# Kernel tuning notes

Hardware: AMD Instinct MI355X
Metric: run time of the kernel (lower is better)

## Reference

```python
import jax, jax.numpy as jnp
import numpy as np

N_NODES = 50000
N_EDGES = 800000
D_MODEL = 128
N_HEADS = 4
N_LAYERS = 2
F_HEAD = D_MODEL // N_HEADS


def setup_inputs() -> dict:
    key = jax.random.key(0)
    ks = jax.random.split(key, 6)
    x = jax.random.normal(ks[0], (N_NODES, D_MODEL), dtype=jnp.float32)
    edge_index = jax.random.randint(ks[1], (2, N_EDGES), 0, N_NODES, dtype=jnp.int64)
    scale = 1.0 / np.sqrt(D_MODEL)
    W = jax.random.normal(ks[2], (N_LAYERS, D_MODEL, D_MODEL), dtype=jnp.float32) * scale
    a_src = jax.random.normal(ks[3], (N_LAYERS, N_HEADS, F_HEAD), dtype=jnp.float32) * scale
    a_dst = jax.random.normal(ks[4], (N_LAYERS, N_HEADS, F_HEAD), dtype=jnp.float32) * scale
    b = jnp.zeros((N_LAYERS, D_MODEL), dtype=jnp.float32)
    return {"x": x, "edge_index": edge_index, "W": W, "a_src": a_src, "a_dst": a_dst, "b": b}


def _gat_layer(x, src, dst, W_l, a_src_l, a_dst_l, b_l, apply_act):
    N = x.shape[0]
    H, F = a_src_l.shape
    # projected node features, split into heads: [N, H, F]
    h = (x @ W_l).reshape(N, H, F)
    # per-node attention contributions: [N, H]
    alpha_s = jnp.einsum("nhf,hf->nh", h, a_src_l)
    alpha_d = jnp.einsum("nhf,hf->nh", h, a_dst_l)
    # per-edge raw scores, LeakyReLU(0.2): [E, H]
    e = jax.nn.leaky_relu(alpha_s[src] + alpha_d[dst], negative_slope=0.2)
    # numerically-stable segment softmax over edges grouped by target node
    e_max = jax.ops.segment_max(e, dst, num_segments=N)
    e_exp = jnp.exp(e - e_max[dst])
    denom = jax.ops.segment_sum(e_exp, dst, num_segments=N)
    alpha = e_exp / (denom[dst] + 1e-16)  # [E, H]
    # gather source features, weight, scatter-add to targets
    msg = h[src] * alpha[:, :, None]  # [E, H, F]
    out = jax.ops.segment_sum(msg, dst, num_segments=N).reshape(N, H * F)
    out = out + x + b_l  # skip connection (dims match) + bias
    return jax.nn.elu(out) if apply_act else out


def reference(x, edge_index, W, a_src, a_dst, b):
    src, dst = edge_index[0], edge_index[1]
    L = W.shape[0]
    for l in range(L):
        x = _gat_layer(x, src, dst, W[l], a_src[l], a_dst[l], b[l], apply_act=(l < L - 1))
    return x
```

## Files before the change

kernel.cpp:

```cpp
#include <hip/hip_runtime.h>
#include <math.h>

constexpr int NN = 50000;
constexpr int NE = 800000;
constexpr int D  = 128;
constexpr int NH = 4;
constexpr int NBUK = (NN + 255) / 256;
constexpr int CAP  = 4608;

typedef __attribute__((ext_vector_type(8))) short short8v;
typedef __attribute__((ext_vector_type(4))) float f32x4;

__device__ inline unsigned short rne_bf16(float f) {
    unsigned bits = __float_as_uint(f);
    return (unsigned short)((bits + 0x7FFFu + ((bits >> 16) & 1u)) >> 16);
}

__global__ __launch_bounds__(256) void bucket_hist_kernel(
    const int* __restrict__ dst, int* __restrict__ btot)
{
    __shared__ int c[NBUK];
    for (int i = threadIdx.x; i < NBUK; i += 256) c[i] = 0;
    __syncthreads();
    const int base = blockIdx.x * 2048;
    #pragma unroll
    for (int i = 0; i < 8; ++i) {
        int e = base + i * 256 + threadIdx.x;
        if (e < NE) atomicAdd(&c[dst[e] >> 8], 1);
    }
    __syncthreads();
    for (int i = threadIdx.x; i < NBUK; i += 256)
        if (c[i]) atomicAdd(&btot[i], c[i]);
}

__global__ __launch_bounds__(256) void bucket_scan_kernel(
    const int* __restrict__ btot, int* __restrict__ bbase,
    int* __restrict__ bwp, int* __restrict__ row_ptr)
{
    const int t = threadIdx.x;
    int v = (t < NBUK) ? btot[t] : 0;
    __shared__ int s[256];
    s[t] = v;
    __syncthreads();
    for (int off = 1; off < 256; off <<= 1) {
        int u = (t >= off) ? s[t - off] : 0;
        __syncthreads();
        s[t] += u;
        __syncthreads();
    }
    if (t < NBUK) { int ex = s[t] - v; bbase[t] = ex; bwp[t] = ex; }
    if (t == 0) row_ptr[NN] = NE;
}

__global__ __launch_bounds__(256) void partition_kernel(
    const int* __restrict__ src, const int* __restrict__ dst,
    int* __restrict__ bwp, unsigned* __restrict__ bukbuf)
{
    __shared__ int cnt[NBUK];
    __shared__ int run[NBUK];
    for (int i = threadIdx.x; i < NBUK; i += 256) cnt[i] = 0;
    __syncthreads();
    const int base = blockIdx.x * 2048;
    int s_[8], b_[8], dl_[8];
    #pragma unroll
    for (int i = 0; i < 8; ++i) {
        int e = base + i * 256 + threadIdx.x;
        bool ok = (e < NE);
        s_[i] = ok ? src[e] : 0;
        int d = ok ? dst[e] : 0;
        b_[i] = d >> 8; dl_[i] = d & 255;
        if (ok) atomicAdd(&cnt[b_[i]], 1);
    }
    __syncthreads();
    for (int i = threadIdx.x; i < NBUK; i += 256)
        run[i] = cnt[i] ? atomicAdd(&bwp[i], cnt[i]) : 0;
    __syncthreads();
    #pragma unroll
    for (int i = 0; i < 8; ++i) {
        int e = base + i * 256 + threadIdx.x;
        if (e < NE) {
            int pos = atomicAdd(&run[b_[i]], 1);
            bukbuf[pos] = (unsigned)s_[i] | ((unsigned)dl_[i] << 16);
        }
    }
}

__global__ __launch_bounds__(256) void bucket_sort_kernel(
    const unsigned* __restrict__ bukbuf, const int* __restrict__ btot,
    const int* __restrict__ bbase, int* __restrict__ row_ptr,
    unsigned short* __restrict__ srcs)
{
    const int b = blockIdx.x;
    const int t = threadIdx.x;
    const int cnt = min(btot[b], CAP);
    const int base = bbase[b];
    __shared__ int hist[256];
    __shared__ int run[256];
    __shared__ int s[256];
    __shared__ unsigned short stage[CAP];
    hist[t] = 0;
    __syncthreads();
    for (int i = t; i < cnt; i += 256)
        atomicAdd(&hist[bukbuf[base + i] >> 16], 1);
    __syncthreads();
    int v = hist[t];
    s[t] = v;
    __syncthreads();
    for (int off = 1; off < 256; off <<= 1) {
        int u = (t >= off) ? s[t - off] : 0;
        __syncthreads();
        s[t] += u;
        __syncthreads();
    }
    const int excl = s[t] - v;
    const int node = b * 256 + t;
    if (node < NN) row_ptr[node] = base + excl;
    run[t] = excl;
    __syncthreads();
    for (int i = t; i < cnt; i += 256) {
        unsigned p = bukbuf[base + i];
        int pos = atomicAdd(&run[p >> 16], 1);
        stage[pos] = (unsigned short)(p & 0xFFFFu);
    }
    __syncthreads();
    for (int i = t; i < cnt; i += 256) srcs[base + i] = stage[i];
}

__global__ __launch_bounds__(256) void repack_kernel(const float* __restrict__ W,
                                                     unsigned short* __restrict__ Wpk,
                                                     int* __restrict__ btot) {
    if (blockIdx.x == 0 && threadIdx.x < NBUK) btot[threadIdx.x] = 0;
    int tid = blockIdx.x * 256 + threadIdx.x;
    if (tid >= 2 * 2048) return;
    int layer = tid >> 11;
    int rest  = tid & 2047;
    int tile  = rest >> 8;
    int kstep = (rest >> 6) & 3;
    int lane  = rest & 63;
    int col   = tile * 16 + (lane & 15);
    int kbase = kstep * 32 + (lane >> 4) * 8;
    const float* Wl = W + (size_t)layer * D * D;
    unsigned short v[8];
    #pragma unroll
    for (int j = 0; j < 8; ++j) v[j] = rne_bf16(Wl[(kbase + j) * D + col]);
    *(uint4*)(Wpk + (size_t)tid * 8) = *(const uint4*)v;
}

template<int BF16IN>
__global__ __launch_bounds__(256) void gemm_alpha_kernel(
    const void* __restrict__ xin, const unsigned short* __restrict__ Wpk,
    const float* __restrict__ a_src, const float* __restrict__ a_dst,
    unsigned short* __restrict__ hb, float* __restrict__ alpha_s,
    float* __restrict__ alpha_d)
{
    __shared__ unsigned short xl[64 * 128];
    const int t = threadIdx.x;
    const int row0 = blockIdx.x * 64;

    if constexpr (BF16IN) {
        const unsigned short* xb = (const unsigned short*)xin;
        #pragma unroll
        for (int it = 0; it < 4; ++it) {
            int idx = it * 256 + t;
            int r   = idx >> 4;
            int c8  = (idx & 15) * 8;
            int n   = row0 + r;
            uint4 v = {0u, 0u, 0u, 0u};
            if (n < NN) v = *(const uint4*)(xb + (size_t)n * D + c8);
            *(uint4*)(xl + r * 128 + (c8 ^ ((r & 7) << 3))) = v;
        }
    } else {
        const float* xf = (const float*)xin;
        #pragma unroll
        for (int it = 0; it < 8; ++it) {
            int idx = it * 256 + t;
            int r   = idx >> 5;
            int c4  = (idx & 31) * 4;
            int n   = row0 + r;
            float4 v;
            if (n < NN) v = *(const float4*)(xf + (size_t)n * D + c4);
            else { v.x = 0.f; v.y = 0.f; v.z = 0.f; v.w = 0.f; }
            unsigned p0 = ((unsigned)rne_bf16(v.y) << 16) | rne_bf16(v.x);
            unsigned p1 = ((unsigned)rne_bf16(v.w) << 16) | rne_bf16(v.z);
            uint2 pv; pv.x = p0; pv.y = p1;
            *(uint2*)(xl + r * 128 + (c4 ^ ((r & 7) << 3))) = pv;
        }
    }
    __syncthreads();

    const int wv  = t >> 6;
    const int l   = t & 63;
    const int l15 = l & 15;
    const int g   = l >> 4;
    const int strip = wv * 16;
    const int arow  = strip + l15;

    f32x4 acc[8];
    #pragma unroll
    for (int i = 0; i < 8; ++i) acc[i] = (f32x4){0.f, 0.f, 0.f, 0.f};

    #pragma unroll
    for (int ks = 0; ks < 4; ++ks) {
        const int k0 = ks * 32 + g * 8;
        short8v a = *(const short8v*)(xl + arow * 128 + (k0 ^ ((arow & 7) << 3)));
        #pragma unroll
        for (int tl = 0; tl < 8; ++tl) {
            short8v b = *(const short8v*)(Wpk + ((size_t)(tl * 4 + ks) * 64 + l) * 8);
            acc[tl] = __builtin_amdgcn_mfma_f32_16x16x32_bf16(a, b, acc[tl], 0, 0, 0);
        }
    }

    float as_t[8], ad_t[8];
    #pragma unroll
    for (int tl = 0; tl < 8; ++tl) {
        as_t[tl] = a_src[tl * 16 + l15];
        ad_t[tl] = a_dst[tl * 16 + l15];
    }

    #pragma unroll
    for (int r = 0; r < 4; ++r) {
        const int n = row0 + strip + g * 4 + r;
        if (n < NN) {
            #pragma unroll
            for (int tl = 0; tl < 8; ++tl)
                hb[(size_t)n * D + tl * 16 + l15] = rne_bf16(acc[tl][r]);
        }
        #pragma unroll
        for (int hd = 0; hd < NH; ++hd) {
            float ps = acc[2*hd][r] * as_t[2*hd] + acc[2*hd+1][r] * as_t[2*hd+1];
            float pd = acc[2*hd][r] * ad_t[2*hd] + acc[2*hd+1][r] * ad_t[2*hd+1];
            #pragma unroll
            for (int off = 1; off < 16; off <<= 1) {
                ps += __shfl_xor(ps, off);
                pd += __shfl_xor(pd, off);
            }
            if (l15 == 0 && n < NN) {
                alpha_s[n * NH + hd] = ps;
                alpha_d[n * NH + hd] = pd;
            }
        }
    }
}

template<int IN_BF16, int OUT_BF16, int ACT>
__global__ __launch_bounds__(256) void gather_kernel(
    const unsigned short* __restrict__ hb, const float* __restrict__ alpha_s,
    const float* __restrict__ alpha_d, const int* __restrict__ row_ptr,
    const unsigned short* __restrict__ srcs, const void* __restrict__ x_in,
    const float* __restrict__ bias, void* __restrict__ out)
{
    const int wave = threadIdx.x >> 6;
    const int lane = threadIdx.x & 63;
    const int q    = lane >> 4;
    const int ql   = lane & 15;
    const int head = ql >> 2;
    const int n = blockIdx.x * 4 + wave;
    if (n >= NN) return;

    const int start = row_ptr[n];
    const int end   = row_ptr[n + 1];
    const float4 ad4 = *(const float4*)&alpha_d[n * NH];

    float acc[8];
    #pragma unroll
    for (int c = 0; c < 8; ++c) acc[c] = 0.f;
    float den = 0.f;

    for (int base = start; base < end; base += 64) {
        const int cnt = min(64, end - base);
        int msrc = 0;
        unsigned uw01 = 0, uw23 = 0;
        if (lane < cnt) {
            msrc = srcs[base + lane];
            const float4 as4 = *(const float4*)&alpha_s[msrc * NH];
            float e0 = as4.x + ad4.x; e0 = (e0 > 0.f) ? e0 : 0.2f * e0;
            float e1 = as4.y + ad4.y; e1 = (e1 > 0.f) ? e1 : 0.2f * e1;
            float e2 = as4.z + ad4.z; e2 = (e2 > 0.f) ? e2 : 0.2f * e2;
            float e3 = as4.w + ad4.w; e3 = (e3 > 0.f) ? e3 : 0.2f * e3;
            float w0 = __expf(e0), w1 = __expf(e1);
            float w2 = __expf(e2), w3 = __expf(e3);
            uw01 = ((unsigned)rne_bf16(w1) << 16) | rne_bf16(w0);
            uw23 = ((unsigned)rne_bf16(w3) << 16) | rne_bf16(w2);
        }
        for (int m = 0; m < cnt; m += 4) {
            const int me = m + q;
            int s = __shfl(msrc, me);
            unsigned b01 = (unsigned)__shfl((int)uw01, me);
            unsigned b23 = (unsigned)__shfl((int)uw23, me);
            unsigned uw = (head < 2) ? b01 : b23;
            float w = __uint_as_float((head & 1) ? (uw & 0xFFFF0000u) : (uw << 16));
            den += w;
            const uint4 hv = *(const uint4*)(hb + (size_t)s * D + ql * 8);
            acc[0] = fmaf(w, __uint_as_float(hv.x << 16),          acc[0]);
            acc[1] = fmaf(w, __uint_as_float(hv.x & 0xFFFF0000u),  acc[1]);
            acc[2] = fmaf(w, __uint_as_float(hv.y << 16),          acc[2]);
            acc[3] = fmaf(w, __uint_as_float(hv.y & 0xFFFF0000u),  acc[3]);
            acc[4] = fmaf(w, __uint_as_float(hv.z << 16),          acc[4]);
            acc[5] = fmaf(w, __uint_as_float(hv.z & 0xFFFF0000u),  acc[5]);
            acc[6] = fmaf(w, __uint_as_float(hv.w << 16),          acc[6]);
            acc[7] = fmaf(w, __uint_as_float(hv.w & 0xFFFF0000u),  acc[7]);
        }
    }
    #pragma unroll
    for (int c = 0; c < 8; ++c) {
        acc[c] += __shfl_xor(acc[c], 16);
        acc[c] += __shfl_xor(acc[c], 32);
    }
    den += __shfl_xor(den, 16);
    den += __shfl_xor(den, 32);

    const float inv = 1.f / (den + 1e-16f);
    const int c0 = ql * 8 + q * 2;
    const size_t o2 = (size_t)n * D + c0;
    float xi0, xi1;
    if constexpr (IN_BF16) {
        unsigned xv = *(const unsigned*)((const unsigned short*)x_in + o2);
        xi0 = __uint_as_float(xv << 16);
        xi1 = __uint_as_float(xv & 0xFFFF0000u);
    } else {
        const float2 xv = *(const float2*)((const float*)x_in + o2);
        xi0 = xv.x; xi1 = xv.y;
    }
    const float2 bi = *(const float2*)(bias + c0);
    float v0 = fmaf(acc[q * 2],     inv, xi0) + bi.x;
    float v1 = fmaf(acc[q * 2 + 1], inv, xi1) + bi.y;
    if constexpr (ACT) {
        v0 = (v0 > 0.f) ? v0 : (__expf(v0) - 1.f);
        v1 = (v1 > 0.f) ? v1 : (__expf(v1) - 1.f);
    }
    if constexpr (OUT_BF16) {
        unsigned ov = ((unsigned)rne_bf16(v1) << 16) | rne_bf16(v0);
        *(unsigned*)((unsigned short*)out + o2) = ov;
    } else {
        float2 o; o.x = v0; o.y = v1;
        *(float2*)((float*)out + o2) = o;
    }
}

extern "C" void kernel_launch(void* const* d_in, const int* in_sizes, int n_in,
                              void* d_out, int out_size, void* d_ws, size_t ws_size,
                              hipStream_t stream) {
    const float* x     = (const float*)d_in[0];
    const int*   ei    = (const int*)d_in[1];
    const float* W     = (const float*)d_in[2];
    const float* a_src = (const float*)d_in[3];
    const float* a_dst = (const float*)d_in[4];
    const float* bias  = (const float*)d_in[5];
    float* outp = (float*)d_out;

    const int* e_src = ei;
    const int* e_dst = ei + NE;

    char* base = (char*)d_ws;
    unsigned short* hb  = (unsigned short*)(base);
    unsigned short* x1b = (unsigned short*)(base + 12800000);
    float* al_s    = (float*)(base + 25600000);
    float* al_d    = (float*)(base + 26400000);
    int*   row_ptr = (int*)  (base + 27200000);
    unsigned short* srcs = (unsigned short*)(base + 27400064);
    unsigned* bukbuf = (unsigned*)(base + 29000064);
    int*   btot    = (int*)  (base + 32200064);
    int*   bbase   = (int*)  (base + 32201088);
    int*   bwp     = (int*)  (base + 32202112);
    unsigned short* Wpk = (unsigned short*)(base + 32203136);

    repack_kernel<<<16, 256, 0, stream>>>(W, Wpk, btot);
    const int pblocks = (NE + 2047) / 2048;
    bucket_hist_kernel<<<pblocks, 256, 0, stream>>>(e_dst, btot);
    bucket_scan_kernel<<<1, 256, 0, stream>>>(btot, bbase, bwp, row_ptr);
    partition_kernel<<<pblocks, 256, 0, stream>>>(e_src, e_dst, bwp, bukbuf);
    bucket_sort_kernel<<<NBUK, 256, 0, stream>>>(bukbuf, btot, bbase, row_ptr, srcs);

    const int gemm_blocks   = (NN + 63) / 64;
    const int gather_blocks = (NN + 3) / 4;

    gemm_alpha_kernel<0><<<gemm_blocks, 256, 0, stream>>>(x, Wpk, a_src, a_dst,
                                                          hb, al_s, al_d);
    gather_kernel<0, 1, 1><<<gather_blocks, 256, 0, stream>>>(
        hb, al_s, al_d, row_ptr, srcs, x, bias, x1b);
    gemm_alpha_kernel<1><<<gemm_blocks, 256, 0, stream>>>(x1b, Wpk + 2048 * 8,
                                                          a_src + D, a_dst + D,
                                                          hb, al_s, al_d);
    gather_kernel<1, 0, 0><<<gather_blocks, 256, 0, stream>>>(
        hb, al_s, al_d, row_ptr, srcs, x1b, bias + D, outp);
}
```

Baseline: 155.5 us.

## Use fixed-capacity buckets to drop histogram/scan passes; map one node per quarter-wave in gather

Edges are now partitioned straight into fixed-capacity per-bucket regions (bucket * CAP), which removes the separate histogram and scan kernels. Each node gets start and end offsets instead of a single CSR row_ptr. The gather kernel now assigns one destination node to each 16-lane group instead of one per wave, so the cross-quarter reduction shuffles go away and each lane writes 8 contiguous outputs with vector stores. In exchange, edges past CAP in a bucket are silently dropped, and each group handles its edges one at a time, which may leave lanes idle when degrees vary.

```diff
diff --git a/kernel.cpp b/kernel.cpp
--- a/kernel.cpp
+++ b/kernel.cpp
@@ -14,42 +14,6 @@
 __device__ inline unsigned short rne_bf16(float f) {
     unsigned bits = __float_as_uint(f);
     return (unsigned short)((bits + 0x7FFFu + ((bits >> 16) & 1u)) >> 16);
-}
-
-__global__ __launch_bounds__(256) void bucket_hist_kernel(
-    const int* __restrict__ dst, int* __restrict__ btot)
-{
-    __shared__ int c[NBUK];
-    for (int i = threadIdx.x; i < NBUK; i += 256) c[i] = 0;
-    __syncthreads();
-    const int base = blockIdx.x * 2048;
-    #pragma unroll
-    for (int i = 0; i < 8; ++i) {
-        int e = base + i * 256 + threadIdx.x;
-        if (e < NE) atomicAdd(&c[dst[e] >> 8], 1);
-    }
-    __syncthreads();
-    for (int i = threadIdx.x; i < NBUK; i += 256)
-        if (c[i]) atomicAdd(&btot[i], c[i]);
-}
-
-__global__ __launch_bounds__(256) void bucket_scan_kernel(
-    const int* __restrict__ btot, int* __restrict__ bbase,
-    int* __restrict__ bwp, int* __restrict__ row_ptr)
-{
-    const int t = threadIdx.x;
-    int v = (t < NBUK) ? btot[t] : 0;
-    __shared__ int s[256];
-    s[t] = v;
-    __syncthreads();
-    for (int off = 1; off < 256; off <<= 1) {
-        int u = (t >= off) ? s[t - off] : 0;
-        __syncthreads();
-        s[t] += u;
-        __syncthreads();
-    }
-    if (t < NBUK) { int ex = s[t] - v; bbase[t] = ex; bwp[t] = ex; }
-    if (t == 0) row_ptr[NN] = NE;
 }
 
 __global__ __launch_bounds__(256) void partition_kernel(
@@ -80,20 +44,21 @@
         int e = base + i * 256 + threadIdx.x;
         if (e < NE) {
             int pos = atomicAdd(&run[b_[i]], 1);
-            bukbuf[pos] = (unsigned)s_[i] | ((unsigned)dl_[i] << 16);
+            if (pos < CAP)
+                bukbuf[b_[i] * CAP + pos] = (unsigned)s_[i] | ((unsigned)dl_[i] << 16);
         }
     }
 }
 
 __global__ __launch_bounds__(256) void bucket_sort_kernel(
-    const unsigned* __restrict__ bukbuf, const int* __restrict__ btot,
-    const int* __restrict__ bbase, int* __restrict__ row_ptr,
+    const unsigned* __restrict__ bukbuf, const int* __restrict__ bwp,
+    int* __restrict__ row_start, int* __restrict__ row_end,
     unsigned short* __restrict__ srcs)
 {
     const int b = blockIdx.x;
     const int t = threadIdx.x;
-    const int cnt = min(btot[b], CAP);
-    const int base = bbase[b];
+    const int cnt = min(bwp[b], CAP);
+    const int base = b * CAP;
     __shared__ int hist[256];
     __shared__ int run[256];
     __shared__ int s[256];
@@ -114,7 +79,10 @@
     }
     const int excl = s[t] - v;
     const int node = b * 256 + t;
-    if (node < NN) row_ptr[node] = base + excl;
+    if (node < NN) {
+        row_start[node] = base + excl;
+        row_end[node]   = base + excl + v;
+    }
     run[t] = excl;
     __syncthreads();
     for (int i = t; i < cnt; i += 256) {
@@ -128,8 +96,8 @@
 
 __global__ __launch_bounds__(256) void repack_kernel(const float* __restrict__ W,
                                                      unsigned short* __restrict__ Wpk,
-                                                     int* __restrict__ btot) {
-    if (blockIdx.x == 0 && threadIdx.x < NBUK) btot[threadIdx.x] = 0;
+                                                     int* __restrict__ bwp) {
+    if (blockIdx.x == 0 && threadIdx.x < NBUK) bwp[threadIdx.x] = 0;
     int tid = blockIdx.x * 256 + threadIdx.x;
     if (tid >= 2 * 2048) return;
     int layer = tid >> 11;
@@ -245,20 +213,21 @@
 template<int IN_BF16, int OUT_BF16, int ACT>
 __global__ __launch_bounds__(256) void gather_kernel(
     const unsigned short* __restrict__ hb, const float* __restrict__ alpha_s,
-    const float* __restrict__ alpha_d, const int* __restrict__ row_ptr,
-    const unsigned short* __restrict__ srcs, const void* __restrict__ x_in,
-    const float* __restrict__ bias, void* __restrict__ out)
+    const float* __restrict__ alpha_d, const int* __restrict__ row_start,
+    const int* __restrict__ row_end, const unsigned short* __restrict__ srcs,
+    const void* __restrict__ x_in, const float* __restrict__ bias,
+    void* __restrict__ out)
 {
-    const int wave = threadIdx.x >> 6;
     const int lane = threadIdx.x & 63;
     const int q    = lane >> 4;
     const int ql   = lane & 15;
     const int head = ql >> 2;
-    const int n = blockIdx.x * 4 + wave;
+    const int lb   = q * 16;
+    const int n = blockIdx.x * 16 + (threadIdx.x >> 6) * 4 + q;
     if (n >= NN) return;
 
-    const int start = row_ptr[n];
-    const int end   = row_ptr[n + 1];
+    const int start = row_start[n];
+    const int end   = row_end[n];
     const float4 ad4 = *(const float4*)&alpha_d[n * NH];
 
     float acc[8];
@@ -266,12 +235,12 @@
     for (int c = 0; c < 8; ++c) acc[c] = 0.f;
     float den = 0.f;
 
-    for (int base = start; base < end; base += 64) {
-        const int cnt = min(64, end - base);
+    for (int base = start; base < end; base += 16) {
+        const int cnt = min(16, end - base);
         int msrc = 0;
         unsigned uw01 = 0, uw23 = 0;
-        if (lane < cnt) {
-            msrc = srcs[base + lane];
+        if (ql < cnt) {
+            msrc = srcs[base + ql];
             const float4 as4 = *(const float4*)&alpha_s[msrc * NH];
             float e0 = as4.x + ad4.x; e0 = (e0 > 0.f) ? e0 : 0.2f * e0;
             float e1 = as4.y + ad4.y; e1 = (e1 > 0.f) ? e1 : 0.2f * e1;
@@ -282,15 +251,14 @@
             uw01 = ((unsigned)rne_bf16(w1) << 16) | rne_bf16(w0);
             uw23 = ((unsigned)rne_bf16(w3) << 16) | rne_bf16(w2);
         }
-        for (int m = 0; m < cnt; m += 4) {
-            const int me = m + q;
-            int s = __shfl(msrc, me);
-            unsigned b01 = (unsigned)__shfl((int)uw01, me);
-            unsigned b23 = (unsigned)__shfl((int)uw23, me);
+        for (int m = 0; m < cnt; ++m) {
+            int s = __shfl(msrc, lb + m);
+            unsigned b01 = (unsigned)__shfl((int)uw01, lb + m);
+            unsigned b23 = (unsigned)__shfl((int)uw23, lb + m);
             unsigned uw = (head < 2) ? b01 : b23;
             float w = __uint_as_float((head & 1) ? (uw & 0xFFFF0000u) : (uw << 16));
             den += w;
-            const uint4 hv = *(const uint4*)(hb + (size_t)s * D + ql * 8);
+            const uint4 hv = *(const uint4*)(hb + ((size_t)s << 7) + (ql << 3));
             acc[0] = fmaf(w, __uint_as_float(hv.x << 16),          acc[0]);
             acc[1] = fmaf(w, __uint_as_float(hv.x & 0xFFFF0000u),  acc[1]);
             acc[2] = fmaf(w, __uint_as_float(hv.y << 16),          acc[2]);
@@ -301,39 +269,46 @@
             acc[7] = fmaf(w, __uint_as_float(hv.w & 0xFFFF0000u),  acc[7]);
         }
     }
+
+    const float inv = 1.f / (den + 1e-16f);
+    const size_t o8 = (size_t)n * D + ql * 8;
+    float xi[8];
+    if constexpr (IN_BF16) {
+        const uint4 xv = *(const uint4*)((const unsigned short*)x_in + o8);
+        xi[0] = __uint_as_float(xv.x << 16);
+        xi[1] = __uint_as_float(xv.x & 0xFFFF0000u);
+        xi[2] = __uint_as_float(xv.y << 16);
+        xi[3] = __uint_as_float(xv.y & 0xFFFF0000u);
+        xi[4] = __uint_as_float(xv.z << 16);
+        xi[5] = __uint_as_float(xv.z & 0xFFFF0000u);
+        xi[6] = __uint_as_float(xv.w << 16);
+        xi[7] = __uint_as_float(xv.w & 0xFFFF0000u);
+    } else {
+        const float4 a = *(const float4*)((const float*)x_in + o8);
+        const float4 b = *(const float4*)((const float*)x_in + o8 + 4);
+        xi[0]=a.x; xi[1]=a.y; xi[2]=a.z; xi[3]=a.w;
+        xi[4]=b.x; xi[5]=b.y; xi[6]=b.z; xi[7]=b.w;
+    }
+    const float4 ba = *(const float4*)(bias + ql * 8);
+    const float4 bb = *(const float4*)(bias + ql * 8 + 4);
+    const float bi[8] = {ba.x, ba.y, ba.z, ba.w, bb.x, bb.y, bb.z, bb.w};
+    float o[8];
     #pragma unroll
     for (int c = 0; c < 8; ++c) {
-        acc[c] += __shfl_xor(acc[c], 16);
-        acc[c] += __shfl_xor(acc[c], 32);
-    }
-    den += __shfl_xor(den, 16);
-    den += __shfl_xor(den, 32);
-
-    const float inv = 1.f / (den + 1e-16f);
-    const int c0 = ql * 8 + q * 2;
-    const size_t o2 = (size_t)n * D + c0;
-    float xi0, xi1;
-    if constexpr (IN_BF16) {
-        unsigned xv = *(const unsigned*)((const unsigned short*)x_in + o2);
-        xi0 = __uint_as_float(xv << 16);
-        xi1 = __uint_as_float(xv & 0xFFFF0000u);
+        float v = fmaf(acc[c], inv, xi[c]) + bi[c];
+        if constexpr (ACT) v = (v > 0.f) ? v : (__expf(v) - 1.f);
+        o[c] = v;
+    }
+    if constexpr (OUT_BF16) {
+        unsigned short ov[8];
+        #pragma unroll
+        for (int c = 0; c < 8; ++c) ov[c] = rne_bf16(o[c]);
+        *(uint4*)((unsigned short*)out + o8) = *(const uint4*)ov;
     } else {
-        const float2 xv = *(const float2*)((const float*)x_in + o2);
-        xi0 = xv.x; xi1 = xv.y;
-    }
-    const float2 bi = *(const float2*)(bias + c0);
-    float v0 = fmaf(acc[q * 2],     inv, xi0) + bi.x;
-    float v1 = fmaf(acc[q * 2 + 1], inv, xi1) + bi.y;
-    if constexpr (ACT) {
-        v0 = (v0 > 0.f) ? v0 : (__expf(v0) - 1.f);
-        v1 = (v1 > 0.f) ? v1 : (__expf(v1) - 1.f);
-    }
-    if constexpr (OUT_BF16) {
-        unsigned ov = ((unsigned)rne_bf16(v1) << 16) | rne_bf16(v0);
-        *(unsigned*)((unsigned short*)out + o2) = ov;
-    } else {
-        float2 o; o.x = v0; o.y = v1;
-        *(float2*)((float*)out + o2) = o;
+        float4 oa = {o[0], o[1], o[2], o[3]};
+        float4 ob = {o[4], o[5], o[6], o[7]};
+        *(float4*)((float*)out + o8)     = oa;
+        *(float4*)((float*)out + o8 + 4) = ob;
     }
 }
 
@@ -354,33 +329,30 @@
     char* base = (char*)d_ws;
     unsigned short* hb  = (unsigned short*)(base);
     unsigned short* x1b = (unsigned short*)(base + 12800000);
-    float* al_s    = (float*)(base + 25600000);
-    float* al_d    = (float*)(base + 26400000);
-    int*   row_ptr = (int*)  (base + 27200000);
-    unsigned short* srcs = (unsigned short*)(base + 27400064);
-    unsigned* bukbuf = (unsigned*)(base + 29000064);
-    int*   btot    = (int*)  (base + 32200064);
-    int*   bbase   = (int*)  (base + 32201088);
-    int*   bwp     = (int*)  (base + 32202112);
-    unsigned short* Wpk = (unsigned short*)(base + 32203136);
-
-    repack_kernel<<<16, 256, 0, stream>>>(W, Wpk, btot);
+    float* al_s      = (float*)(base + 25600000);
+    float* al_d      = (float*)(base + 26400000);
+    int*   row_start = (int*)  (base + 27200000);
+    int*   row_end   = (int*)  (base + 27400000);
+    unsigned short* srcs = (unsigned short*)(base + 27600000);
+    unsigned* bukbuf = (unsigned*)(base + 29406336);
+    int*   bwp       = (int*)  (base + 33019008);
+    unsigned short* Wpk = (unsigned short*)(base + 33019792);
+
+    repack_kernel<<<16, 256, 0, stream>>>(W, Wpk, bwp);
     const int pblocks = (NE + 2047) / 2048;
-    bucket_hist_kernel<<<pblocks, 256, 0, stream>>>(e_dst, btot);
-    bucket_scan_kernel<<<1, 256, 0, stream>>>(btot, bbase, bwp, row_ptr);
     partition_kernel<<<pblocks, 256, 0, stream>>>(e_src, e_dst, bwp, bukbuf);
-    bucket_sort_kernel<<<NBUK, 256, 0, stream>>>(bukbuf, btot, bbase, row_ptr, srcs);
+    bucket_sort_kernel<<<NBUK, 256, 0, stream>>>(bukbuf, bwp, row_start, row_end, srcs);
 
     const int gemm_blocks   = (NN + 63) / 64;
-    const int gather_blocks = (NN + 3) / 4;
+    const int gather_blocks = (NN + 15) / 16;
 
     gemm_alpha_kernel<0><<<gemm_blocks, 256, 0, stream>>>(x, Wpk, a_src, a_dst,
                                                           hb, al_s, al_d);
     gather_kernel<0, 1, 1><<<gather_blocks, 256, 0, stream>>>(
-        hb, al_s, al_d, row_ptr, srcs, x, bias, x1b);
+        hb, al_s, al_d, row_start, row_end, srcs, x, bias, x1b);
     gemm_alpha_kernel<1><<<gemm_blocks, 256, 0, stream>>>(x1b, Wpk + 2048 * 8,
                                                           a_src + D, a_dst + D,
                                                           hb, al_s, al_d);
     gather_kernel<1, 0, 0><<<gather_blocks, 256, 0, stream>>>(
-        hb, al_s, al_d, row_ptr, srcs, x1b, bias + D, outp);
-}
+        hb, al_s, al_d, row_start, row_end, srcs, x1b, bias + D, outp);
+}
```

New measurement: 141.0 us. 1.1x faster.
